# Kernel optimization log

Measured on AMD Instinct MI355X. Metric: run time of the kernel, lower is better.

The kernel has to match this reference:

```python
import jax, jax.numpy as jnp
import numpy as np

B, T, V, H = 16, 128, 32000, 768
P = H // 2
NBOW = 64
PAD = 0
EPS = 0.05     # label smoothing
TAU = 0.07
W_CE, W_AL, W_BOW, W_DIV, W_VAR = 1.0, 0.5, 0.2, 0.1, 0.05
BOW_IDS = jnp.arange(NBOW, dtype=jnp.int32) * 500  # registered buffer bow_indices_tensor


def _ln(x, g, b):
    m = jnp.mean(x, axis=-1, keepdims=True)
    v = jnp.mean((x - m) ** 2, axis=-1, keepdims=True)
    return (x - m) / jnp.sqrt(v + 1e-5) * g + b


def _l2norm(x):
    return x / jnp.maximum(jnp.linalg.norm(x, axis=-1, keepdims=True), 1e-12)


def _proj(x, g, bn, W1, b1, W2, b2):
    h = _ln(x, g, bn)
    h = jax.nn.gelu(h @ W1 + b1, approximate=False)  # torch nn.GELU default = exact
    return h @ W2 + b2


def setup_inputs() -> dict:
    key = jax.random.key(0)
    ks = jax.random.split(key, 12)
    s = 0.02
    return {
        "logits": jax.random.normal(ks[0], (B, T, V), dtype=jnp.float32),
        "labels": jax.random.randint(ks[1], (B, T), 0, V, dtype=jnp.int32),
        "attention_mask": jnp.ones((B, T), dtype=jnp.int32),
        "encoder_features": jax.random.normal(ks[2], (B, H), dtype=jnp.float32),
        "decoder_hidden": jax.random.normal(ks[3], (B, T, H), dtype=jnp.float32),
        "ln_g_e": jnp.ones((H,), jnp.float32), "ln_b_e": jnp.zeros((H,), jnp.float32),
        "W1_e": jax.random.normal(ks[4], (H, P), jnp.float32) * s, "b1_e": jnp.zeros((P,), jnp.float32),
        "W2_e": jax.random.normal(ks[5], (P, P), jnp.float32) * s, "b2_e": jnp.zeros((P,), jnp.float32),
        "ln_g_t": jnp.ones((H,), jnp.float32), "ln_b_t": jnp.zeros((H,), jnp.float32),
        "W1_t": jax.random.normal(ks[6], (H, P), jnp.float32) * s, "b1_t": jnp.zeros((P,), jnp.float32),
        "W2_t": jax.random.normal(ks[7], (P, P), jnp.float32) * s, "b2_t": jnp.zeros((P,), jnp.float32),
        "W_bow": jax.random.normal(ks[8], (H, NBOW), jnp.float32) * s, "b_bow": jnp.zeros((NBOW,), jnp.float32),
    }


def _forward(logits, labels, attention_mask, encoder_features, decoder_hidden,
             ln_g_e, ln_b_e, W1_e, b1_e, W2_e, b2_e,
             ln_g_t, ln_b_t, W1_t, b1_t, W2_t, b2_t,
             W_bow, b_bow):
    # --- label-smoothed CE over valid (non-pad, non -100) tokens ---
    valid = (labels != PAD) & (labels != -100)                      # (B,T)
    lab = jnp.clip(labels, 0, V - 1)
    lp = jax.nn.log_softmax(logits, axis=-1)                        # (B,T,V)
    lp_lab = jnp.take_along_axis(lp, lab[..., None], axis=-1)[..., 0]
    tok_loss = -((1.0 - EPS) * lp_lab + (EPS / V) * lp.sum(-1))     # smooth target = (1-eps) at label + eps/V everywhere
    vf = valid.astype(jnp.float32)
    ce = (tok_loss * vf).sum() / jnp.maximum(vf.sum(), 1.0)

    # --- contrastive alignment (InfoNCE both ways) ---
    m = attention_mask[..., None].astype(jnp.float32)               # (B,T,1)
    pooled = (decoder_hidden * m).sum(1) / jnp.maximum(m.sum(1), 1.0)
    z_e = _l2norm(_proj(encoder_features, ln_g_e, ln_b_e, W1_e, b1_e, W2_e, b2_e))
    z_t = _l2norm(_proj(pooled, ln_g_t, ln_b_t, W1_t, b1_t, W2_t, b2_t))
    sim = (z_e @ z_t.T) / TAU                                       # (B,B)
    li = -jnp.diag(jax.nn.log_softmax(sim, axis=-1)).mean()
    lj = -jnp.diag(jax.nn.log_softmax(sim.T, axis=-1)).mean()
    align = 0.5 * (li + lj)

    # --- BoW BCE: target[b,i] = any valid token of row b equals bow id i ---
    match = (lab[:, :, None] == BOW_IDS[None, None, :]) & valid[:, :, None]
    bow_t = match.any(axis=1).astype(jnp.float32)                   # (B,NBOW)
    bl = encoder_features @ W_bow + b_bow
    bce = jnp.mean(jnp.maximum(bl, 0.0) - bl * bow_t + jnp.log1p(jnp.exp(-jnp.abs(bl))))

    # --- diversity: mean |off-diagonal cosine sim| of encoder features ---
    nf = _l2norm(encoder_features)
    sm = nf @ nf.T
    off = 1.0 - jnp.eye(B, dtype=jnp.float32)
    div = (jnp.abs(sm) * off).sum() / (B * B - B)

    # --- variance: mean exp(-var_dim) (torch.var uses ddof=1) ---
    fvar = jnp.var(encoder_features, axis=0, ddof=1)
    var_l = jnp.mean(jnp.exp(-fvar))

    return W_CE * ce + W_AL * align + W_BOW * bce + W_DIV * div + W_VAR * var_l


def reference(logits, labels, attention_mask, encoder_features, decoder_hidden,
              ln_g_e, ln_b_e, W1_e, b1_e, W2_e, b2_e,
              ln_g_t, ln_b_t, W1_t, b1_t, W2_t, b2_t,
              W_bow, b_bow):
    return _forward(logits, labels, attention_mask, encoder_features, decoder_hidden,
                    ln_g_e, ln_b_e, W1_e, b1_e, W2_e, b2_e,
                    ln_g_t, ln_b_t, W1_t, b1_t, W2_t, b2_t,
                    W_bow, b_bow)
```

## Files before the change

kernel.cpp:

```cpp
#include <hip/hip_runtime.h>
#include <math.h>

#define BB 16
#define TT 128
#define VV 32000
#define HH 768
#define PP 384
#define NBOWD 64
#define EPS_LS 0.05f
#define TAUC 0.07f
#define NCE (BB * TT)
#define SMALLB 101

typedef float fvec4 __attribute__((ext_vector_type(4)));

__device__ __forceinline__ float blockReduceSum256(float v, float* sh) {
  int tid = threadIdx.x;
  sh[tid] = v;
  __syncthreads();
  for (int s = 128; s > 0; s >>= 1) {
    if (tid < s) sh[tid] += sh[tid + s];
    __syncthreads();
  }
  float r = sh[0];
  __syncthreads();
  return r;
}

__global__ __launch_bounds__(256) void fused_main(
    const float* __restrict__ logits, const int* __restrict__ labels, const int* __restrict__ amask,
    const float* __restrict__ enc, const float* __restrict__ dh,
    const float* __restrict__ g_e, const float* __restrict__ be_, const float* __restrict__ W1e,
    const float* __restrict__ b1e, const float* __restrict__ W2e, const float* __restrict__ b2e,
    const float* __restrict__ g_t, const float* __restrict__ bt_, const float* __restrict__ W1t,
    const float* __restrict__ b1t, const float* __restrict__ W2t, const float* __restrict__ b2t,
    const float* __restrict__ W_bow, const float* __restrict__ b_bow,
    float* __restrict__ tok, float* __restrict__ vfs,
    float* __restrict__ ze, float* __restrict__ zt,
    float* __restrict__ bowp, float* __restrict__ divp, float* __restrict__ var_p) {
  __shared__ float smem[1792];
  int tid = threadIdx.x;
  int blk = blockIdx.x;

  if (blk < NCE) {
    int row = blk;
    const float* x = logits + (size_t)row * VV;
    const fvec4* x4 = (const fvec4*)x;
    float s0 = 0.f, s1 = 0.f, s2 = 0.f, s3 = 0.f;
    float sxa = 0.f, sxb = 0.f;
#pragma unroll 3
    for (int it = 0; it < 15; ++it) {
      int base = (it << 9) + tid;
      fvec4 v0 = __builtin_nontemporal_load(x4 + base);
      fvec4 v1 = __builtin_nontemporal_load(x4 + base + 256);
      sxa += (v0.x + v0.y) + (v0.z + v0.w);
      sxb += (v1.x + v1.y) + (v1.z + v1.w);
      s0 += __expf(v0.x) + __expf(v0.y);
      s1 += __expf(v0.z) + __expf(v0.w);
      s2 += __expf(v1.x) + __expf(v1.y);
      s3 += __expf(v1.z) + __expf(v1.w);
    }
    {
      int base = (15 << 9) + tid;
      fvec4 v0 = __builtin_nontemporal_load(x4 + base);
      sxa += (v0.x + v0.y) + (v0.z + v0.w);
      s0 += __expf(v0.x) + __expf(v0.y);
      s1 += __expf(v0.z) + __expf(v0.w);
      if (tid < 64) {
        fvec4 v1 = __builtin_nontemporal_load(x4 + base + 256);
        sxb += (v1.x + v1.y) + (v1.z + v1.w);
        s2 += __expf(v1.x) + __expf(v1.y);
        s3 += __expf(v1.z) + __expf(v1.w);
      }
    }
    float s = (s0 + s1) + (s2 + s3);
    float sx = sxa + sxb;

    float* sa = smem;
    float* sb = smem + 256;
    sa[tid] = s; sb[tid] = sx;
    __syncthreads();
    for (int o = 128; o > 0; o >>= 1) {
      if (tid < o) { sa[tid] += sa[tid + o]; sb[tid] += sb[tid + o]; }
      __syncthreads();
    }
    if (tid == 0) {
      float L = logf(sa[0]);
      float SX = sb[0];
      int lab = labels[row];
      bool valid = (lab != 0) && (lab != -100);
      int lc = lab < 0 ? 0 : (lab > VV - 1 ? VV - 1 : lab);
      float xl = x[lc];
      float lp_lab = xl - L;
      float lp_sum = SX - (float)VV * L;
      float tl = -((1.f - EPS_LS) * lp_lab + (EPS_LS / (float)VV) * lp_sum);
      tok[row] = valid ? tl : 0.f;
      vfs[row] = valid ? 1.f : 0.f;
    }
    return;
  }

  int sblk = blk - NCE;

  if (sblk < 32) {
    float* xs = smem;
    float* hs = smem + 768;
    float* red = smem + 1152;
    float* mf = smem + 1408;
    float* mden = smem + 1536;
    bool is_t = sblk >= BB;
    int b = sblk & (BB - 1);
    const float *g, *bb_, *W1, *b1, *W2, *b2;
    float* zout;
    if (is_t) { g = g_t; bb_ = bt_; W1 = W1t; b1 = b1t; W2 = W2t; b2 = b2t; zout = zt; }
    else      { g = g_e; bb_ = be_; W1 = W1e; b1 = b1e; W2 = W2e; b2 = b2e; zout = ze; }

    if (is_t) {
      if (tid < TT) mf[tid] = (float)amask[b * TT + tid];
      __syncthreads();
      if (tid == 0) {
        float sum = 0.f;
        for (int t = 0; t < TT; t++) sum += mf[t];
        mden[0] = fmaxf(sum, 1.f);
      }
      __syncthreads();
      const float* dbase = dh + (size_t)b * TT * HH;
      for (int h = tid; h < HH; h += 256) {
        const float* db = dbase + h;
        float a0 = 0.f, a1 = 0.f, a2 = 0.f, a3 = 0.f;
#pragma unroll 8
        for (int t = 0; t < TT; t += 4) {
          a0 += db[(t + 0) * HH] * mf[t + 0];
          a1 += db[(t + 1) * HH] * mf[t + 1];
          a2 += db[(t + 2) * HH] * mf[t + 2];
          a3 += db[(t + 3) * HH] * mf[t + 3];
        }
        xs[h] = ((a0 + a1) + (a2 + a3)) / mden[0];
      }
    } else {
      for (int k = tid; k < HH; k += 256) xs[k] = enc[b * HH + k];
    }
    __syncthreads();

    float s1 = 0.f, s2 = 0.f;
    for (int k = tid; k < HH; k += 256) { float v = xs[k]; s1 += v; s2 += v * v; }
    s1 = blockReduceSum256(s1, red);
    s2 = blockReduceSum256(s2, red);
    float mean = s1 / (float)HH;
    float var = s2 / (float)HH - mean * mean;
    float rstd = rsqrtf(var + 1e-5f);
    for (int k = tid; k < HH; k += 256) xs[k] = (xs[k] - mean) * rstd * g[k] + bb_[k];
    __syncthreads();

    for (int j = tid; j < PP; j += 256) {
      float a0 = 0.f, a1 = 0.f;
#pragma unroll 8
      for (int k = 0; k < HH; k += 2) {
        a0 += xs[k] * W1[k * PP + j];
        a1 += xs[k + 1] * W1[(k + 1) * PP + j];
      }
      float acc = b1[j] + a0 + a1;
      hs[j] = 0.5f * acc * (1.f + erff(acc * 0.70710678118654752440f));
    }
    __syncthreads();
    for (int j = tid; j < PP; j += 256) {
      float a0 = 0.f, a1 = 0.f;
#pragma unroll 8
      for (int k = 0; k < PP; k += 2) {
        a0 += hs[k] * W2[k * PP + j];
        a1 += hs[k + 1] * W2[(k + 1) * PP + j];
      }
      xs[j] = b2[j] + a0 + a1;
    }
    __syncthreads();
    float sq = 0.f;
    for (int j = tid; j < PP; j += 256) { float v = xs[j]; sq += v * v; }
    sq = blockReduceSum256(sq, red);
    float inv = 1.f / fmaxf(sqrtf(sq), 1e-12f);
    for (int j = tid; j < PP; j += 256) zout[b * PP + j] = xs[j] * inv;
    return;
  }

  if (sblk < 96) {
    int bb = sblk - 32;
    int b = bb >> 2, kq = bb & 3;
    int iw = tid & 63, ks = tid >> 6;
    const float* er = enc + b * HH;
    int k0 = kq * 192 + ks * 48;
    float acc = 0.f;
#pragma unroll 8
    for (int k = 0; k < 48; ++k) acc += er[k0 + k] * W_bow[(k0 + k) * NBOWD + iw];
    smem[ks * 64 + iw] = acc;
    __syncthreads();
    if (tid < 64) bowp[bb * 64 + tid] = smem[tid] + smem[64 + tid] + smem[128 + tid] + smem[192 + tid];
    return;
  }

  if (sblk < 100) {
    int kq = sblk - 96;
    int i = tid >> 4, j = tid & 15;
    const float* a = enc + i * HH + kq * 192;
    const float* c = enc + j * HH + kq * 192;
    float a0 = 0.f, a1 = 0.f;
#pragma unroll 8
    for (int k = 0; k < 192; k += 2) {
      a0 += a[k] * c[k];
      a1 += a[k + 1] * c[k + 1];
    }
    divp[kq * 256 + tid] = a0 + a1;
    return;
  }

  {
    float vsum = 0.f;
    for (int d = tid; d < HH; d += 256) {
      float a1 = 0.f, a2 = 0.f;
#pragma unroll
      for (int b = 0; b < BB; b++) { float v = enc[b * HH + d]; a1 += v; a2 += v * v; }
      float mean = a1 / (float)BB;
      float vr = (a2 - (float)BB * mean * mean) / (float)(BB - 1);
      vsum += __expf(-vr);
    }
    float r = blockReduceSum256(vsum, smem);
    if (tid == 0) var_p[0] = r / (float)HH;
  }
}

__global__ __launch_bounds__(256) void finalize2(
    const float* __restrict__ tok, const float* __restrict__ vfs,
    const float* __restrict__ ze, const float* __restrict__ zt,
    const float* __restrict__ bowp, const float* __restrict__ divp, const float* __restrict__ var_p,
    const int* __restrict__ labels, const float* __restrict__ b_bow,
    float* __restrict__ out) {
  __shared__ float sh[256];
  __shared__ float smat[256];
  __shared__ float misc[40];
  __shared__ int flags[BB * NBOWD];
  int tid = threadIdx.x;

  for (int i = tid; i < BB * NBOWD; i += 256) flags[i] = 0;
  __syncthreads();
  for (int i = tid; i < BB * TT; i += 256) {
    int lab = labels[i];
    if (lab != 0 && lab != -100) {
      int lc = lab < 0 ? 0 : (lab > VV - 1 ? VV - 1 : lab);
      if (lc % 500 == 0) {
        int iw = lc / 500;
        if (iw < NBOWD) flags[(i >> 7) * NBOWD + iw] = 1;
      }
    }
  }

  float tsum = 0.f, csum = 0.f;
  for (int i = tid; i < BB * TT; i += 256) { tsum += tok[i]; csum += vfs[i]; }
  float ce_sum = blockReduceSum256(tsum, sh);
  float ce_cnt = blockReduceSum256(csum, sh);

  {
    int i = tid >> 4, j = tid & 15;
    const float* a = ze + i * PP;
    const float* c = zt + j * PP;
    float a0 = 0.f, a1 = 0.f;
#pragma unroll 8
    for (int k = 0; k < PP; k += 2) { a0 += a[k] * c[k]; a1 += a[k + 1] * c[k + 1]; }
    smat[tid] = (a0 + a1) * (1.f / TAUC);
  }
  __syncthreads();
  if (tid < 32) {
    bool isrow = tid < 16;
    int r = tid & 15;
    float mx = -1e30f;
    for (int j = 0; j < 16; j++) { float v = isrow ? smat[r * 16 + j] : smat[j * 16 + r]; mx = fmaxf(mx, v); }
    float se = 0.f;
    for (int j = 0; j < 16; j++) { float v = isrow ? smat[r * 16 + j] : smat[j * 16 + r]; se += __expf(v - mx); }
    misc[tid] = smat[r * 17] - mx - logf(se);
  }
  __syncthreads();
  float align;
  if (tid == 0) {
    float li = 0.f, lj = 0.f;
    for (int r = 0; r < 16; r++) { li += misc[r]; lj += misc[16 + r]; }
    misc[33] = 0.5f * (-(li / 16.f) - (lj / 16.f));
  }
  __syncthreads();
  align = misc[33];
  __syncthreads();

  float bsum = 0.f;
  for (int e = tid; e < BB * NBOWD; e += 256) {
    int b = e >> 6, iw = e & 63;
    float bl = b_bow[iw] + bowp[(b * 4 + 0) * 64 + iw] + bowp[(b * 4 + 1) * 64 + iw]
             + bowp[(b * 4 + 2) * 64 + iw] + bowp[(b * 4 + 3) * 64 + iw];
    float tgt = (float)flags[e];
    bsum += fmaxf(bl, 0.f) - bl * tgt + log1pf(__expf(-fabsf(bl)));
  }
  float bce = blockReduceSum256(bsum, sh) / (float)(BB * NBOWD);

  smat[tid] = divp[tid] + divp[256 + tid] + divp[512 + tid] + divp[768 + tid];
  __syncthreads();
  float contrib = 0.f;
  {
    int i = tid >> 4, j = tid & 15;
    if (i != j) {
      float ni = fmaxf(sqrtf(smat[i * 17]), 1e-12f);
      float nj = fmaxf(sqrtf(smat[j * 17]), 1e-12f);
      contrib = fabsf(smat[tid]) / (ni * nj);
    }
  }
  float divs = blockReduceSum256(contrib, sh) / (float)(BB * BB - BB);

  if (tid == 0) {
    float ce = ce_sum / fmaxf(ce_cnt, 1.f);
    out[0] = 1.0f * ce + 0.5f * align + 0.2f * bce + 0.1f * divs + 0.05f * var_p[0];
  }
}

extern "C" void kernel_launch(void* const* d_in, const int* in_sizes, int n_in,
                              void* d_out, int out_size, void* d_ws, size_t ws_size,
                              hipStream_t stream) {
  const float* logits = (const float*)d_in[0];
  const int* labels   = (const int*)d_in[1];
  const int* amask    = (const int*)d_in[2];
  const float* enc    = (const float*)d_in[3];
  const float* dh     = (const float*)d_in[4];
  const float* g_e    = (const float*)d_in[5];
  const float* be_    = (const float*)d_in[6];
  const float* W1e    = (const float*)d_in[7];
  const float* b1e    = (const float*)d_in[8];
  const float* W2e    = (const float*)d_in[9];
  const float* b2e    = (const float*)d_in[10];
  const float* g_t    = (const float*)d_in[11];
  const float* bt_    = (const float*)d_in[12];
  const float* W1t    = (const float*)d_in[13];
  const float* b1t    = (const float*)d_in[14];
  const float* W2t    = (const float*)d_in[15];
  const float* b2t    = (const float*)d_in[16];
  const float* W_bow  = (const float*)d_in[17];
  const float* b_bow  = (const float*)d_in[18];

  float* f     = (float*)d_ws;
  float* tok   = f;
  float* vfs   = f + 2048;
  float* ze    = f + 4096;
  float* zt    = f + 10240;
  float* bowp  = f + 16384;
  float* divp  = f + 20480;
  float* var_p = f + 21504;

  fused_main<<<NCE + SMALLB, 256, 0, stream>>>(
      logits, labels, amask, enc, dh,
      g_e, be_, W1e, b1e, W2e, b2e,
      g_t, bt_, W1t, b1t, W2t, b2t,
      W_bow, b_bow, tok, vfs, ze, zt, bowp, divp, var_p);
  finalize2<<<1, 256, 0, stream>>>(tok, vfs, ze, zt, bowp, divp, var_p, labels, b_bow, (float*)d_out);
}
```

Before: 470.8 us.

## Split CE logit rows into chunks interleaved across blocks, reduce partials in finalize

Each vocab row is split into 25 chunks, and every CE block walks 25 chunks in an interleaved order across rows. Each block does a wave-level shuffle reduction and writes per-wave float2 partials (sum of exp, sum of x) without block barriers or shared memory. The single-block finalize kernel then sums 100 partials per row, gathers the label logit and computes the smoothed CE. This removes the block-wide reduction and syncs from the streaming kernel. In exchange, the one-block finalize now does much more serial work (204800 partial reads plus 2048 scattered label gathers), which may become a tail bottleneck.

Measured after the change: 541.0 us. 14.9% more time.

```diff
diff --git a/kernel.cpp b/kernel.cpp
--- a/kernel.cpp
+++ b/kernel.cpp
@@ -11,6 +11,9 @@
 #define TAUC 0.07f
 #define NCE (BB * TT)
 #define SMALLB 101
+#define NCHUNK 25
+#define CHUNK_F4 320
+#define ROW_F4 8000
 
 typedef float fvec4 __attribute__((ext_vector_type(4)));
 
@@ -35,7 +38,7 @@
     const float* __restrict__ g_t, const float* __restrict__ bt_, const float* __restrict__ W1t,
     const float* __restrict__ b1t, const float* __restrict__ W2t, const float* __restrict__ b2t,
     const float* __restrict__ W_bow, const float* __restrict__ b_bow,
-    float* __restrict__ tok, float* __restrict__ vfs,
+    float2* __restrict__ pw,
     float* __restrict__ ze, float* __restrict__ zt,
     float* __restrict__ bowp, float* __restrict__ divp, float* __restrict__ var_p) {
   __shared__ float smem[1792];
@@ -43,59 +46,31 @@
   int blk = blockIdx.x;
 
   if (blk < NCE) {
-    int row = blk;
-    const float* x = logits + (size_t)row * VV;
-    const fvec4* x4 = (const fvec4*)x;
-    float s0 = 0.f, s1 = 0.f, s2 = 0.f, s3 = 0.f;
-    float sxa = 0.f, sxb = 0.f;
-#pragma unroll 3
-    for (int it = 0; it < 15; ++it) {
-      int base = (it << 9) + tid;
-      fvec4 v0 = __builtin_nontemporal_load(x4 + base);
-      fvec4 v1 = __builtin_nontemporal_load(x4 + base + 256);
-      sxa += (v0.x + v0.y) + (v0.z + v0.w);
-      sxb += (v1.x + v1.y) + (v1.z + v1.w);
-      s0 += __expf(v0.x) + __expf(v0.y);
-      s1 += __expf(v0.z) + __expf(v0.w);
-      s2 += __expf(v1.x) + __expf(v1.y);
-      s3 += __expf(v1.z) + __expf(v1.w);
-    }
-    {
-      int base = (15 << 9) + tid;
-      fvec4 v0 = __builtin_nontemporal_load(x4 + base);
-      sxa += (v0.x + v0.y) + (v0.z + v0.w);
-      s0 += __expf(v0.x) + __expf(v0.y);
-      s1 += __expf(v0.z) + __expf(v0.w);
-      if (tid < 64) {
-        fvec4 v1 = __builtin_nontemporal_load(x4 + base + 256);
-        sxb += (v1.x + v1.y) + (v1.z + v1.w);
-        s2 += __expf(v1.x) + __expf(v1.y);
-        s3 += __expf(v1.z) + __expf(v1.w);
-      }
-    }
-    float s = (s0 + s1) + (s2 + s3);
-    float sx = sxa + sxb;
-
-    float* sa = smem;
-    float* sb = smem + 256;
-    sa[tid] = s; sb[tid] = sx;
-    __syncthreads();
-    for (int o = 128; o > 0; o >>= 1) {
-      if (tid < o) { sa[tid] += sa[tid + o]; sb[tid] += sb[tid + o]; }
-      __syncthreads();
-    }
-    if (tid == 0) {
-      float L = logf(sa[0]);
-      float SX = sb[0];
-      int lab = labels[row];
-      bool valid = (lab != 0) && (lab != -100);
-      int lc = lab < 0 ? 0 : (lab > VV - 1 ? VV - 1 : lab);
-      float xl = x[lc];
-      float lp_lab = xl - L;
-      float lp_sum = SX - (float)VV * L;
-      float tl = -((1.f - EPS_LS) * lp_lab + (EPS_LS / (float)VV) * lp_sum);
-      tok[row] = valid ? tl : 0.f;
-      vfs[row] = valid ? 1.f : 0.f;
+    int wv = tid >> 6, lane = tid & 63;
+    const fvec4* x4 = (const fvec4*)logits;
+#pragma unroll 2
+    for (int i = 0; i < NCHUNK; ++i) {
+      int c = i * NCE + blk;
+      int row = c / NCHUNK;
+      int sub = c - row * NCHUNK;
+      const fvec4* cp = x4 + (size_t)row * ROW_F4 + sub * CHUNK_F4;
+      fvec4 v0 = __builtin_nontemporal_load(cp + tid);
+      float s_l = (__expf(v0.x) + __expf(v0.y)) + (__expf(v0.z) + __expf(v0.w));
+      float sx_l = (v0.x + v0.y) + (v0.z + v0.w);
+      if ((i & 3) == wv) {
+        fvec4 v1 = __builtin_nontemporal_load(cp + 256 + lane);
+        s_l += (__expf(v1.x) + __expf(v1.y)) + (__expf(v1.z) + __expf(v1.w));
+        sx_l += (v1.x + v1.y) + (v1.z + v1.w);
+      }
+#pragma unroll
+      for (int m = 32; m > 0; m >>= 1) {
+        s_l += __shfl_xor(s_l, m, 64);
+        sx_l += __shfl_xor(sx_l, m, 64);
+      }
+      if (lane == 0) {
+        float2 p; p.x = s_l; p.y = sx_l;
+        pw[c * 4 + wv] = p;
+      }
     }
     return;
   }
@@ -227,7 +202,7 @@
 }
 
 __global__ __launch_bounds__(256) void finalize2(
-    const float* __restrict__ tok, const float* __restrict__ vfs,
+    const float* __restrict__ logits, const float2* __restrict__ pw,
     const float* __restrict__ ze, const float* __restrict__ zt,
     const float* __restrict__ bowp, const float* __restrict__ divp, const float* __restrict__ var_p,
     const int* __restrict__ labels, const float* __restrict__ b_bow,
@@ -252,7 +227,21 @@
   }
 
   float tsum = 0.f, csum = 0.f;
-  for (int i = tid; i < BB * TT; i += 256) { tsum += tok[i]; csum += vfs[i]; }
+  for (int r = tid; r < BB * TT; r += 256) {
+    const float2* pr = pw + (size_t)r * (NCHUNK * 4);
+    float S = 0.f, SX = 0.f;
+#pragma unroll 4
+    for (int j = 0; j < NCHUNK * 4; ++j) { S += pr[j].x; SX += pr[j].y; }
+    int lab = labels[r];
+    bool valid = (lab != 0) && (lab != -100);
+    int lc = lab < 0 ? 0 : (lab > VV - 1 ? VV - 1 : lab);
+    float xl = logits[(size_t)r * VV + lc];
+    float L = logf(S);
+    float lp_lab = xl - L;
+    float lp_sum = SX - (float)VV * L;
+    float tl = -((1.f - EPS_LS) * lp_lab + (EPS_LS / (float)VV) * lp_sum);
+    if (valid) { tsum += tl; csum += 1.f; }
+  }
   float ce_sum = blockReduceSum256(tsum, sh);
   float ce_cnt = blockReduceSum256(csum, sh);
 
@@ -338,19 +327,18 @@
   const float* W_bow  = (const float*)d_in[17];
   const float* b_bow  = (const float*)d_in[18];
 
-  float* f     = (float*)d_ws;
-  float* tok   = f;
-  float* vfs   = f + 2048;
-  float* ze    = f + 4096;
-  float* zt    = f + 10240;
-  float* bowp  = f + 16384;
-  float* divp  = f + 20480;
-  float* var_p = f + 21504;
+  float* f      = (float*)d_ws;
+  float2* pw    = (float2*)d_ws;
+  float* ze     = f + 409600;
+  float* zt     = f + 415744;
+  float* bowp   = f + 421888;
+  float* divp   = f + 425984;
+  float* var_p  = f + 427008;
 
   fused_main<<<NCE + SMALLB, 256, 0, stream>>>(
       logits, labels, amask, enc, dh,
       g_e, be_, W1e, b1e, W2e, b2e,
       g_t, bt_, W1t, b1t, W2t, b2t,
-      W_bow, b_bow, tok, vfs, ze, zt, bowp, divp, var_p);
-  finalize2<<<1, 256, 0, stream>>>(tok, vfs, ze, zt, bowp, divp, var_p, labels, b_bow, (float*)d_out);
+      W_bow, b_bow, pw, ze, zt, bowp, divp, var_p);
+  finalize2<<<1, 256, 0, stream>>>(logits, pw, ze, zt, bowp, divp, var_p, labels, b_bow, (float*)d_out);
 }
```
